# Kernel tuning notes

Hardware: AMD Instinct MI355X
Metric: run time of the kernel (lower is better)

The kernel has to match this reference:

```python
import jax, jax.numpy as jnp
import numpy as np

BS, NS, NSTEP = 128, 1024, 8
IN_DIM, HID, MLP = 768, 512, 512
NEG = -100000.0


def setup_inputs() -> dict:
    key = jax.random.key(0)
    ks = jax.random.split(key, 12)
    s_h = 1.0 / np.sqrt(HID)
    s_cat = 1.0 / np.sqrt(HID + IN_DIM)
    s_m = 1.0 / np.sqrt(MLP)
    # gumbel noise implements Categorical sampling as argmax(logits + gumbel)
    u = jax.random.uniform(ks[9], (NSTEP, BS, NS), jnp.float32, 1e-7, 1.0 - 1e-7)
    return {
        "target_emb": jax.random.normal(ks[0], (BS, IN_DIM), jnp.float32),
        "ctx_emb": jax.random.normal(ks[1], (BS, NS, IN_DIM), jnp.float32),
        "target_len": jax.random.randint(ks[2], (BS,), 1, 32),
        "ctx_len": jax.random.randint(ks[3], (BS,), NSTEP, NS + 1),
        "n_step": NSTEP,
        "W_ih": jax.random.normal(ks[4], (4 * HID, IN_DIM), jnp.float32) * s_h,
        "W_hh": jax.random.normal(ks[5], (4 * HID, HID), jnp.float32) * s_h,
        "b_ih": jnp.zeros((4 * HID,), jnp.float32),
        "b_hh": jnp.zeros((4 * HID,), jnp.float32),
        "W1c": jax.random.normal(ks[6], (MLP, IN_DIM), jnp.float32) * s_cat,
        "W1h": jax.random.normal(ks[7], (MLP, HID), jnp.float32) * s_cat,
        "b1": jnp.zeros((MLP,), jnp.float32),
        "w2": jax.random.normal(ks[8], (MLP,), jnp.float32) * s_m,
        "b2": jnp.zeros((), jnp.float32),
        "gumbel": -jnp.log(-jnp.log(u)),
    }


def reference(target_emb, ctx_emb, target_len, ctx_len, n_step,
              W_ih, W_hh, b_ih, b_hh, W1c, W1h, b1, w2, b2, gumbel):
    bs, ns, in_dim = ctx_emb.shape
    hid = W_hh.shape[1]
    # mlp1 split: ctx part is constant across steps (concat([ctx, h]) @ W1^T = ctx@W1c^T + h@W1h^T)
    ctx_part = jnp.einsum('bnd,md->bnm', ctx_emb, W1c) + b1  # [bs, ns, mlp]
    mask0 = jnp.where(jnp.arange(ns)[None, :] >= ctx_len[:, None], NEG, 0.0).astype(jnp.float32)
    h0 = jnp.zeros((bs, hid), jnp.float32)
    c0 = jnp.zeros((bs, hid), jnp.float32)
    lp0 = jnp.zeros((bs,), jnp.float32)
    batch_idx = jnp.arange(bs)

    def step(carry, g):
        h, c, mask, x, lp = carry
        # LSTMCell (torch gate order: i, f, g, o); dropout is identity (eval semantics)
        gates = x @ W_ih.T + b_ih + h @ W_hh.T + b_hh
        i_g, f_g, g_g, o_g = jnp.split(gates, 4, axis=-1)
        c_new = jax.nn.sigmoid(f_g) * c + jax.nn.sigmoid(i_g) * jnp.tanh(g_g)
        h_new = jax.nn.sigmoid(o_g) * jnp.tanh(c_new)
        # attention-style MLP score
        pre = ctx_part + (h_new @ W1h.T)[:, None, :]          # [bs, ns, mlp]
        sc = jnp.tanh(pre) @ w2 + b2 + mask                   # [bs, ns]
        # Categorical(probs=softmax(sc)).sample() via Gumbel-argmax
        out = jnp.argmax(sc + g, axis=-1)                     # [bs]
        lp = lp + jnp.take_along_axis(jax.nn.log_softmax(sc, axis=-1), out[:, None], 1)[:, 0]
        mask = mask.at[batch_idx, out].set(NEG)
        x_new = jnp.take_along_axis(ctx_emb, out[:, None, None], axis=1)[:, 0, :]
        return (h_new, c_new, mask, x_new, lp), out

    (h, c, mask, x, log_probs), outputs = jax.lax.scan(
        step, (h0, c0, mask0, target_emb, lp0), gumbel)
    return outputs, log_probs
```

## Files before the change

### kernel.cpp

```cpp
#include <hip/hip_runtime.h>
#include <hip/hip_bf16.h>

#define BSZ 128
#define NSQ 1024
#define NSTEPC 8
#define IND 768
#define HIDD 512
#define G4D 2048
#define MLPD 512
#define NEGV -100000.0f
#define KSGATE 4
#define MSPLIT 4

typedef __attribute__((ext_vector_type(4))) float f32x4;
typedef __attribute__((ext_vector_type(8))) short short8v;

__device__ __forceinline__ void gl16(const unsigned short* g, unsigned short* l) {
  __builtin_amdgcn_global_load_lds(
      (const __attribute__((address_space(1))) unsigned int*)(g),
      (__attribute__((address_space(3))) unsigned int*)(l), 16, 0, 0);
}

__device__ __forceinline__ void split2(float4 f0, float4 f1, short8v& hi, short8v& lo) {
  float fv[8] = {f0.x, f0.y, f0.z, f0.w, f1.x, f1.y, f1.z, f1.w};
#pragma unroll
  for (int j = 0; j < 8; ++j) {
    const unsigned ub = __builtin_bit_cast(unsigned, fv[j]);
    const unsigned hb = ub & 0xFFFF0000u;
    const float lf = fv[j] - __builtin_bit_cast(float, hb);
    hi[j] = (short)(hb >> 16);
    lo[j] = (short)(__builtin_bit_cast(unsigned, lf) >> 16);
  }
}

__device__ __forceinline__ float tanh_fast(float x) {
  x = fminf(fmaxf(x, -15.0f), 15.0f);
  float e = __builtin_amdgcn_exp2f(x * 2.8853900817779268f);
  float r = __builtin_amdgcn_rcpf(e + 1.0f);
  return fmaf(-2.0f, r, 1.0f);
}

__global__ __launch_bounds__(256) void k_prep_w(
    const float* __restrict__ W1c, const float* __restrict__ W_ih,
    const float* __restrict__ W_hh,
    unsigned short* __restrict__ wch, unsigned short* __restrict__ wcl,
    unsigned short* __restrict__ wgh, unsigned short* __restrict__ wgl) {
  int c = blockIdx.x * 256 + threadIdx.x;
  const float* src;
  unsigned short *dh, *dl;
  size_t unit;
  if (c < 49152) {
    const int row = c / 96, wc = c - row * 96;
    const int tile = wc >> 2, c4 = wc & 3;
    const int slot = c4 ^ ((row >> 1) & 3);
    unit = ((size_t)((row >> 7) * 24 + tile) * 128 + (row & 127)) * 4 + slot;
    src = W1c + (size_t)row * IND + wc * 8;
    dh = wch; dl = wcl;
  } else {
    c -= 49152;
    if (c >= 327680) return;
    const int row = c / 160, wc = c - row * 160;
    const int k0 = wc * 8;
    const int tile = wc >> 2, c4 = wc & 3;
    const int slot = c4 ^ ((row >> 1) & 3);
    unit = ((size_t)((row >> 7) * 40 + tile) * 128 + (row & 127)) * 4 + slot;
    src = (k0 < IND) ? (W_ih + (size_t)row * IND + k0)
                     : (W_hh + (size_t)row * HIDD + (k0 - IND));
    dh = wgh; dl = wgl;
  }
  const float4 f0 = *(const float4*)src, f1 = *(const float4*)(src + 4);
  short8v hi, lo;
  split2(f0, f1, hi, lo);
  *(short8v*)(dh + unit * 8) = hi;
  *(short8v*)(dl + unit * 8) = lo;
}

__global__ __launch_bounds__(256) void k_init2(
    const float* __restrict__ te, const int* __restrict__ cl,
    float* __restrict__ mask, float* __restrict__ cst, float* __restrict__ lp,
    unsigned short* __restrict__ xhh, unsigned short* __restrict__ xhl) {
  const int b = blockIdx.x, tid = threadIdx.x;
  const int L = cl[b];
  for (int n = tid; n < NSQ; n += 256) mask[(size_t)b * NSQ + n] = (n >= L) ? NEGV : 0.0f;
  for (int j = tid; j < HIDD; j += 256) cst[(size_t)b * HIDD + j] = 0.0f;
  if (tid == 0) lp[b] = 0.0f;
  if (tid < 160) {
    const int tile = tid >> 2, c4 = tid & 3;
    const int slot = c4 ^ ((b >> 1) & 3);
    const size_t ub = (((size_t)tile * 128 + b) * 4 + slot) * 8;
    short8v hi = {}, lo = {};
    if (tid < 96) {
      const float* s = te + (size_t)b * IND + tid * 8;
      split2(*(const float4*)s, *(const float4*)(s + 4), hi, lo);
    }
    *(short8v*)&xhh[ub] = hi;
    *(short8v*)&xhl[ub] = lo;
  }
}

__global__ __launch_bounds__(256) void k_ctx2(
    const float* __restrict__ ctx,
    const unsigned short* __restrict__ wch, const unsigned short* __restrict__ wcl,
    const float* __restrict__ bias, const int* __restrict__ clen,
    float* __restrict__ cp) {
  __shared__ __align__(16) unsigned short sWh[8192], sWl[8192];
  __shared__ __align__(16) unsigned short sCh[2048], sCl[2048];
  const int i0 = blockIdx.y * 64;
  const int b = i0 >> 10;
  const int nbase = i0 & 1023;
  if (nbase >= clen[b]) return;
  const int m0 = blockIdx.x * 256;
  const int rb0 = blockIdx.x * 2;
  const int tid = threadIdx.x;
  const int lane = tid & 63, wid = tid >> 6;
  const int l15 = lane & 15, l4 = lane >> 4;
  const int crow = tid >> 2, cc4 = tid & 3;
  const int ckread = cc4 ^ ((crow >> 1) & 3);
  const float* csrc = ctx + (size_t)(i0 + crow) * IND + ckread * 8;

  f32x4 acc[4][4] = {};
  for (int t = 0; t < 24; ++t) {
#pragma unroll
    for (int i = 0; i < 8; ++i) {
      const int v = wid * 1024 + i * 4096;
      const int plane = v >> 14;
      const int rem = v & 16383;
      const int rbh = rem >> 13;
      const int offs = (rem & 8191) >> 1;
      const unsigned short* g = (plane ? wcl : wch) +
          ((size_t)((rb0 + rbh) * 24 + t)) * 4096 + offs + lane * 8;
      unsigned short* l = (plane ? sWl : sWh) + rbh * 4096 + offs;
      gl16(g, l);
    }
    {
      const float* s = csrc + t * 32;
      short8v hi, lo;
      split2(*(const float4*)s, *(const float4*)(s + 4), hi, lo);
      *(short8v*)&sCh[tid * 8] = hi;
      *(short8v*)&sCl[tid * 8] = lo;
    }
    __syncthreads();
    short8v ah[4], al[4], bh[4], bl[4];
#pragma unroll
    for (int f = 0; f < 4; ++f) {
      const int rw = wid * 64 + f * 16 + l15;
      const int sw = l4 ^ ((rw >> 1) & 3);
      ah[f] = *(const short8v*)&sWh[rw * 32 + sw * 8];
      al[f] = *(const short8v*)&sWl[rw * 32 + sw * 8];
      const int rc = f * 16 + l15;
      const int sc = l4 ^ ((rc >> 1) & 3);
      bh[f] = *(const short8v*)&sCh[rc * 32 + sc * 8];
      bl[f] = *(const short8v*)&sCl[rc * 32 + sc * 8];
    }
#pragma unroll
    for (int fm = 0; fm < 4; ++fm)
#pragma unroll
      for (int fn = 0; fn < 4; ++fn) {
        acc[fm][fn] = __builtin_amdgcn_mfma_f32_16x16x32_bf16(ah[fm], bh[fn], acc[fm][fn], 0, 0, 0);
        acc[fm][fn] = __builtin_amdgcn_mfma_f32_16x16x32_bf16(ah[fm], bl[fn], acc[fm][fn], 0, 0, 0);
        acc[fm][fn] = __builtin_amdgcn_mfma_f32_16x16x32_bf16(al[fm], bh[fn], acc[fm][fn], 0, 0, 0);
      }
    __syncthreads();
  }
#pragma unroll
  for (int fm = 0; fm < 4; ++fm) {
#pragma unroll
    for (int r = 0; r < 4; ++r) {
      const int m = m0 + wid * 64 + fm * 16 + l4 * 4 + r;
      const float bb = bias[m];
      float* dst = cp + (((size_t)(b * MLPD + m)) << 10) + nbase + l15;
#pragma unroll
      for (int fn = 0; fn < 4; ++fn)
        dst[fn * 16] = acc[fm][fn][r] + bb;
    }
  }
}

__global__ __launch_bounds__(256) void k_gates(
    const unsigned short* __restrict__ xhh, const unsigned short* __restrict__ xhl,
    const unsigned short* __restrict__ wgh, const unsigned short* __restrict__ wgl,
    float* __restrict__ gp) {
  __shared__ __align__(16) unsigned short sAh[4096], sAl[4096], sBh[4096], sBl[4096];
  const int nb = blockIdx.x;
  const int ks = blockIdx.y;
  const int tid = threadIdx.x;
  const int lane = tid & 63, wid = tid >> 6;
  const int wm = wid >> 1, wn = wid & 1;
  const int l15 = lane & 15, l4 = lane >> 4;
  f32x4 acc[4][4] = {};
  for (int t = 0; t < 10; ++t) {
    const int gt = ks * 10 + t;
#pragma unroll
    for (int i = 0; i < 8; ++i) {
      const int v = wid * 1024 + i * 4096;
      const int mm = v >> 13;
      const int offs = (v & 8191) >> 1;
      const unsigned short* g;
      unsigned short* l;
      if (mm == 0)      { g = xhh + (size_t)gt * 4096 + offs; l = sAh + offs; }
      else if (mm == 1) { g = xhl + (size_t)gt * 4096 + offs; l = sAl + offs; }
      else if (mm == 2) { g = wgh + ((size_t)nb * 40 + gt) * 4096 + offs; l = sBh + offs; }
      else              { g = wgl + ((size_t)nb * 40 + gt) * 4096 + offs; l = sBl + offs; }
      gl16(g + lane * 8, l);
    }
    __syncthreads();
    short8v ahv[4], alv[4], bhv[4], blv[4];
#pragma unroll
    for (int f = 0; f < 4; ++f) {
      const int ri = wm * 64 + f * 16 + l15;
      const int sa = l4 ^ ((ri >> 1) & 3);
      ahv[f] = *(const short8v*)&sAh[ri * 32 + sa * 8];
      alv[f] = *(const short8v*)&sAl[ri * 32 + sa * 8];
      const int rn = wn * 64 + f * 16 + l15;
      const int sb = l4 ^ ((rn >> 1) & 3);
      bhv[f] = *(const short8v*)&sBh[rn * 32 + sb * 8];
      blv[f] = *(const short8v*)&sBl[rn * 32 + sb * 8];
    }
#pragma unroll
    for (int fi = 0; fi < 4; ++fi)
#pragma unroll
      for (int fn = 0; fn < 4; ++fn) {
        acc[fi][fn] = __builtin_amdgcn_mfma_f32_16x16x32_bf16(ahv[fi], bhv[fn], acc[fi][fn], 0, 0, 0);
        acc[fi][fn] = __builtin_amdgcn_mfma_f32_16x16x32_bf16(ahv[fi], blv[fn], acc[fi][fn], 0, 0, 0);
        acc[fi][fn] = __builtin_amdgcn_mfma_f32_16x16x32_bf16(alv[fi], bhv[fn], acc[fi][fn], 0, 0, 0);
      }
    __syncthreads();
  }
#pragma unroll
  for (int fi = 0; fi < 4; ++fi) {
#pragma unroll
    for (int r = 0; r < 4; ++r) {
      const int i = wm * 64 + fi * 16 + l4 * 4 + r;
      float* dst = gp + ((size_t)ks * BSZ + i) * G4D + nb * 128 + wn * 64 + l15;
#pragma unroll
      for (int fn = 0; fn < 4; ++fn)
        dst[fn * 16] = acc[fi][fn][r];
    }
  }
}

__global__ __launch_bounds__(512) void k_lstm2(
    const float* __restrict__ gp, const float* __restrict__ b_ih,
    const float* __restrict__ b_hh, const float* __restrict__ W1h,
    float* __restrict__ cst,
    unsigned short* __restrict__ xhh, unsigned short* __restrict__ xhl,
    float* __restrict__ hpp) {
  __shared__ float hs[HIDD];
  const int b = blockIdx.x, j = threadIdx.x;
  float g[4];
#pragma unroll
  for (int q = 0; q < 4; ++q) {
    float s = b_ih[q * HIDD + j] + b_hh[q * HIDD + j];
#pragma unroll
    for (int ks = 0; ks < KSGATE; ++ks)
      s += gp[((size_t)ks * BSZ + b) * G4D + q * HIDD + j];
    g[q] = s;
  }
  const float c_old = cst[(size_t)b * HIDD + j];
  const float ig = 1.0f / (1.0f + expf(-g[0]));
  const float fg = 1.0f / (1.0f + expf(-g[1]));
  const float gg = tanhf(g[2]);
  const float og = 1.0f / (1.0f + expf(-g[3]));
  const float cn = fg * c_old + ig * gg;
  const float hn = og * tanhf(cn);
  cst[(size_t)b * HIDD + j] = cn;
  hs[j] = hn;
  {
    const int tile = 24 + (j >> 5);
    const int c4 = (j >> 3) & 3;
    const int slot = c4 ^ ((b >> 1) & 3);
    const size_t u16i = (((size_t)tile * 128 + b) * 4 + slot) * 8 + (j & 7);
    const unsigned ubh = __builtin_bit_cast(unsigned, hn) & 0xFFFF0000u;
    const float lf = hn - __builtin_bit_cast(float, ubh);
    xhh[u16i] = (unsigned short)(ubh >> 16);
    xhl[u16i] = (unsigned short)(__builtin_bit_cast(unsigned, lf) >> 16);
  }
  __syncthreads();
  const float* wr = W1h + (size_t)j * HIDD;
  float s = 0.0f;
#pragma unroll 4
  for (int k = 0; k < HIDD; k += 4) {
    const float4 h4 = *(const float4*)&hs[k];
    const float4 w4 = *(const float4*)&wr[k];
    s = fmaf(h4.x, w4.x, fmaf(h4.y, w4.y, fmaf(h4.z, w4.z, fmaf(h4.w, w4.w, s))));
  }
  hpp[(size_t)b * HIDD + j] = s;
}

__global__ __launch_bounds__(256) void k_scores(
    const float* __restrict__ cp, const float* __restrict__ hpp,
    const float* __restrict__ w2, const int* __restrict__ clen,
    float* __restrict__ psc) {
  const int mh = blockIdx.x;
  const int b = blockIdx.y;
  const int tid = threadIdx.x;
  __shared__ float hsm[128], wsm[128];
  if (tid < 128) {
    hsm[tid] = hpp[(size_t)b * MLPD + mh * 128 + tid];
    wsm[tid] = w2[mh * 128 + tid];
  }
  __syncthreads();
  const int len = clen[b];
  const int n0 = tid * 4;
  if (n0 >= len) return;
  float ax = 0, ay = 0, az = 0, aw = 0;
  const float* base = cp + ((size_t)b * MLPD + mh * 128) * NSQ + n0;
#pragma unroll 4
  for (int mm = 0; mm < 128; ++mm) {
    const float4 c4 = *(const float4*)(base + (size_t)mm * NSQ);
    const float h = hsm[mm], w = wsm[mm];
    ax = fmaf(tanh_fast(c4.x + h), w, ax);
    ay = fmaf(tanh_fast(c4.y + h), w, ay);
    az = fmaf(tanh_fast(c4.z + h), w, az);
    aw = fmaf(tanh_fast(c4.w + h), w, aw);
  }
  *(float4*)(psc + ((size_t)b * MSPLIT + mh) * NSQ + n0) = make_float4(ax, ay, az, aw);
}

__global__ __launch_bounds__(256) void k_argmax(
    const float* __restrict__ psc, float* __restrict__ mask,
    const float* __restrict__ gum, const float* __restrict__ b2p,
    float* __restrict__ lp, const float* __restrict__ ctx,
    unsigned short* __restrict__ xhh, unsigned short* __restrict__ xhl,
    float* __restrict__ outv, int step) {
  const int b = blockIdx.x, tid = threadIdx.x;
  __shared__ float rv[256], rs[256], rm[256];
  __shared__ int ri[256];
  __shared__ int sel;
  const float b2 = b2p[0];
  const int n0 = tid * 4;
  const float4 m4 = *(const float4*)(mask + (size_t)b * NSQ + n0);
  float sc[4] = {b2 + m4.x, b2 + m4.y, b2 + m4.z, b2 + m4.w};
#pragma unroll
  for (int mh = 0; mh < MSPLIT; ++mh) {
    const float4 p4 = *(const float4*)(psc + ((size_t)b * MSPLIT + mh) * NSQ + n0);
    sc[0] += p4.x; sc[1] += p4.y; sc[2] += p4.z; sc[3] += p4.w;
  }
  const float4 g4 = *(const float4*)(gum + ((size_t)step * BSZ + b) * NSQ + n0);
  const float gv[4] = {g4.x, g4.y, g4.z, g4.w};
  float bestv = -1e30f, bests = 0.0f, msc = -1e30f;
  int bestn = 0;
#pragma unroll
  for (int q = 0; q < 4; ++q) {
    const float v = sc[q] + gv[q];
    if (v > bestv) { bestv = v; bestn = n0 + q; bests = sc[q]; }
    msc = fmaxf(msc, sc[q]);
  }
  rv[tid] = bestv; ri[tid] = bestn; rs[tid] = bests; rm[tid] = msc;
  __syncthreads();
  for (int o = 128; o > 0; o >>= 1) {
    if (tid < o) {
      if (rv[tid + o] > rv[tid] || (rv[tid + o] == rv[tid] && ri[tid + o] < ri[tid])) {
        rv[tid] = rv[tid + o]; ri[tid] = ri[tid + o]; rs[tid] = rs[tid + o];
      }
      rm[tid] = fmaxf(rm[tid], rm[tid + o]);
    }
    __syncthreads();
  }
  const float M = rm[0];
  __syncthreads();
  float se = 0.0f;
#pragma unroll
  for (int q = 0; q < 4; ++q)
    se += __builtin_amdgcn_exp2f((sc[q] - M) * 1.4426950408889634f);
  rm[tid] = se;
  __syncthreads();
  for (int o = 128; o > 0; o >>= 1) {
    if (tid < o) rm[tid] += rm[tid + o];
    __syncthreads();
  }
  if (tid == 0) {
    const int n = ri[0];
    const float lse = M + logf(rm[0]);
    const float nlp = lp[b] + rs[0] - lse;
    lp[b] = nlp;
    mask[(size_t)b * NSQ + n] = NEGV;
    outv[step * BSZ + b] = (float)n;
    if (step == NSTEPC - 1) outv[NSTEPC * BSZ + b] = nlp;
    sel = n;
  }
  __syncthreads();
  const int n = sel;
  if (tid < 96) {
    const float* src = ctx + ((size_t)b * NSQ + n) * IND + tid * 8;
    const int tile = tid >> 2, c4 = tid & 3;
    const int slot = c4 ^ ((b >> 1) & 3);
    const size_t ub = (((size_t)tile * 128 + b) * 4 + slot) * 8;
    short8v hi, lo;
    split2(*(const float4*)src, *(const float4*)(src + 4), hi, lo);
    *(short8v*)&xhh[ub] = hi;
    *(short8v*)&xhl[ub] = lo;
  }
}

extern "C" void kernel_launch(void* const* d_in, const int* in_sizes, int n_in,
                              void* d_out, int out_size, void* d_ws, size_t ws_size,
                              hipStream_t stream) {
  const float* target_emb = (const float*)d_in[0];
  const float* ctx_emb   = (const float*)d_in[1];
  const int*   ctx_len   = (const int*)d_in[3];
  const float* W_ih = (const float*)d_in[5];
  const float* W_hh = (const float*)d_in[6];
  const float* b_ih = (const float*)d_in[7];
  const float* b_hh = (const float*)d_in[8];
  const float* W1c  = (const float*)d_in[9];
  const float* W1h  = (const float*)d_in[10];
  const float* b1   = (const float*)d_in[11];
  const float* w2   = (const float*)d_in[12];
  const float* b2   = (const float*)d_in[13];
  const float* gumbel = (const float*)d_in[14];
  float* out = (float*)d_out;

  float* ws = (float*)d_ws;
  size_t off = 0;
  auto alloc = [&](size_t n) { float* p = ws + off; off += (n + 63) & ~(size_t)63; return p; };

  float* cp   = alloc((size_t)BSZ * MLPD * NSQ);
  float* gp   = alloc((size_t)KSGATE * BSZ * G4D);
  float* hpp  = alloc((size_t)BSZ * MLPD);
  float* psc  = alloc((size_t)BSZ * MSPLIT * NSQ);
  float* mask = alloc((size_t)BSZ * NSQ);
  float* cst  = alloc((size_t)BSZ * HIDD);
  float* lp   = alloc(128);
  unsigned short* wch = (unsigned short*)alloc(196608);
  unsigned short* wcl = (unsigned short*)alloc(196608);
  unsigned short* wgh = (unsigned short*)alloc(1310720);
  unsigned short* wgl = (unsigned short*)alloc(1310720);
  unsigned short* xhh = (unsigned short*)alloc(81920);
  unsigned short* xhl = (unsigned short*)alloc(81920);

  k_prep_w<<<1472, 256, 0, stream>>>(W1c, W_ih, W_hh, wch, wcl, wgh, wgl);
  k_init2<<<BSZ, 256, 0, stream>>>(target_emb, ctx_len, mask, cst, lp, xhh, xhl);
  k_ctx2<<<dim3(2, 2048), 256, 0, stream>>>(ctx_emb, wch, wcl, b1, ctx_len, cp);

  for (int t = 0; t < NSTEPC; ++t) {
    k_gates<<<dim3(16, KSGATE), 256, 0, stream>>>(xhh, xhl, wgh, wgl, gp);
    k_lstm2<<<BSZ, 512, 0, stream>>>(gp, b_ih, b_hh, W1h, cst, xhh, xhl, hpp);
    k_scores<<<dim3(MSPLIT, BSZ), 256, 0, stream>>>(cp, hpp, w2, ctx_len, psc);
    k_argmax<<<BSZ, 256, 0, stream>>>(psc, mask, gumbel, b2, lp, ctx_emb, xhh, xhl, out, t);
  }
}
```

Before: 953.8 us.

## Fuse score and argmax kernels, enlarge ctx GEMM tile, double gate split-K

Merges the per-step score and argmax kernels into one launch. The last of the MSPLIT blocks for each batch row, found with an atomic counter and threadfence, performs the reduction, sampling and mask update. The ctx projection GEMM moves to 512-thread blocks covering 128 context rows, so each W1c tile loaded into LDS is reused twice as much. The gate GEMM split-K factor goes from 4 to 8 for more parallelism, at the cost of more partial sums for the LSTM kernel to reduce. The fusion removes eight launches but relies on correct memory fencing and counter reset.

```diff
diff --git a/kernel.cpp b/kernel.cpp
--- a/kernel.cpp
+++ b/kernel.cpp
@@ -9,7 +9,7 @@
 #define G4D 2048
 #define MLPD 512
 #define NEGV -100000.0f
-#define KSGATE 4
+#define KSGATE 8
 #define MSPLIT 4
 
 typedef __attribute__((ext_vector_type(4))) float f32x4;
@@ -78,12 +78,13 @@
 __global__ __launch_bounds__(256) void k_init2(
     const float* __restrict__ te, const int* __restrict__ cl,
     float* __restrict__ mask, float* __restrict__ cst, float* __restrict__ lp,
+    int* __restrict__ cnt,
     unsigned short* __restrict__ xhh, unsigned short* __restrict__ xhl) {
   const int b = blockIdx.x, tid = threadIdx.x;
   const int L = cl[b];
   for (int n = tid; n < NSQ; n += 256) mask[(size_t)b * NSQ + n] = (n >= L) ? NEGV : 0.0f;
   for (int j = tid; j < HIDD; j += 256) cst[(size_t)b * HIDD + j] = 0.0f;
-  if (tid == 0) lp[b] = 0.0f;
+  if (tid == 0) { lp[b] = 0.0f; cnt[b] = 0; }
   if (tid < 160) {
     const int tile = tid >> 2, c4 = tid & 3;
     const int slot = c4 ^ ((b >> 1) & 3);
@@ -98,21 +99,22 @@
   }
 }
 
-__global__ __launch_bounds__(256) void k_ctx2(
+__global__ __launch_bounds__(512) void k_ctx3(
     const float* __restrict__ ctx,
     const unsigned short* __restrict__ wch, const unsigned short* __restrict__ wcl,
     const float* __restrict__ bias, const int* __restrict__ clen,
     float* __restrict__ cp) {
   __shared__ __align__(16) unsigned short sWh[8192], sWl[8192];
-  __shared__ __align__(16) unsigned short sCh[2048], sCl[2048];
-  const int i0 = blockIdx.y * 64;
-  const int b = i0 >> 10;
+  __shared__ __align__(16) unsigned short sCh[4096], sCl[4096];
+  const int i0 = blockIdx.y * 128;
+  const int b = blockIdx.y >> 3;
   const int nbase = i0 & 1023;
   if (nbase >= clen[b]) return;
   const int m0 = blockIdx.x * 256;
   const int rb0 = blockIdx.x * 2;
   const int tid = threadIdx.x;
   const int lane = tid & 63, wid = tid >> 6;
+  const int wm = wid & 3, wn = wid >> 2;
   const int l15 = lane & 15, l4 = lane >> 4;
   const int crow = tid >> 2, cc4 = tid & 3;
   const int ckread = cc4 ^ ((crow >> 1) & 3);
@@ -121,15 +123,13 @@
   f32x4 acc[4][4] = {};
   for (int t = 0; t < 24; ++t) {
 #pragma unroll
-    for (int i = 0; i < 8; ++i) {
-      const int v = wid * 1024 + i * 4096;
-      const int plane = v >> 14;
-      const int rem = v & 16383;
-      const int rbh = rem >> 13;
-      const int offs = (rem & 8191) >> 1;
-      const unsigned short* g = (plane ? wcl : wch) +
-          ((size_t)((rb0 + rbh) * 24 + t)) * 4096 + offs + lane * 8;
-      unsigned short* l = (plane ? sWl : sWh) + rbh * 4096 + offs;
+    for (int i = 0; i < 4; ++i) {
+      const int s = wid * 4 + i;
+      const int p = s >> 4, q = s & 15;
+      const int rbh = q >> 3;
+      const unsigned short* g = (p ? wcl : wch) +
+          ((size_t)((rb0 + rbh) * 24 + t)) * 4096 + (q & 7) * 512 + lane * 8;
+      unsigned short* l = (p ? sWl : sWh) + q * 512;
       gl16(g, l);
     }
     {
@@ -143,11 +143,11 @@
     short8v ah[4], al[4], bh[4], bl[4];
 #pragma unroll
     for (int f = 0; f < 4; ++f) {
-      const int rw = wid * 64 + f * 16 + l15;
+      const int rw = wm * 64 + f * 16 + l15;
       const int sw = l4 ^ ((rw >> 1) & 3);
       ah[f] = *(const short8v*)&sWh[rw * 32 + sw * 8];
       al[f] = *(const short8v*)&sWl[rw * 32 + sw * 8];
-      const int rc = f * 16 + l15;
+      const int rc = wn * 64 + f * 16 + l15;
       const int sc = l4 ^ ((rc >> 1) & 3);
       bh[f] = *(const short8v*)&sCh[rc * 32 + sc * 8];
       bl[f] = *(const short8v*)&sCl[rc * 32 + sc * 8];
@@ -166,9 +166,9 @@
   for (int fm = 0; fm < 4; ++fm) {
 #pragma unroll
     for (int r = 0; r < 4; ++r) {
-      const int m = m0 + wid * 64 + fm * 16 + l4 * 4 + r;
+      const int m = m0 + wm * 64 + fm * 16 + l4 * 4 + r;
       const float bb = bias[m];
-      float* dst = cp + (((size_t)(b * MLPD + m)) << 10) + nbase + l15;
+      float* dst = cp + (((size_t)(b * MLPD + m)) << 10) + nbase + wn * 64 + l15;
 #pragma unroll
       for (int fn = 0; fn < 4; ++fn)
         dst[fn * 16] = acc[fm][fn][r] + bb;
@@ -188,8 +188,8 @@
   const int wm = wid >> 1, wn = wid & 1;
   const int l15 = lane & 15, l4 = lane >> 4;
   f32x4 acc[4][4] = {};
-  for (int t = 0; t < 10; ++t) {
-    const int gt = ks * 10 + t;
+  for (int t = 0; t < 5; ++t) {
+    const int gt = ks * 5 + t;
 #pragma unroll
     for (int i = 0; i < 8; ++i) {
       const int v = wid * 1024 + i * 4096;
@@ -287,53 +287,59 @@
   hpp[(size_t)b * HIDD + j] = s;
 }
 
-__global__ __launch_bounds__(256) void k_scores(
+__global__ __launch_bounds__(256) void k_scoremax(
     const float* __restrict__ cp, const float* __restrict__ hpp,
     const float* __restrict__ w2, const int* __restrict__ clen,
-    float* __restrict__ psc) {
+    float* __restrict__ psc, int* __restrict__ cnt,
+    float* __restrict__ mask, const float* __restrict__ gum,
+    const float* __restrict__ b2p, float* __restrict__ lp,
+    const float* __restrict__ ctx,
+    unsigned short* __restrict__ xhh, unsigned short* __restrict__ xhl,
+    float* __restrict__ outv, int step) {
   const int mh = blockIdx.x;
   const int b = blockIdx.y;
   const int tid = threadIdx.x;
   __shared__ float hsm[128], wsm[128];
+  __shared__ float rv[256], rs[256], rm[256];
+  __shared__ int ri[256];
+  __shared__ int lastFlag, sel;
+  const int len = clen[b];
   if (tid < 128) {
     hsm[tid] = hpp[(size_t)b * MLPD + mh * 128 + tid];
     wsm[tid] = w2[mh * 128 + tid];
   }
   __syncthreads();
-  const int len = clen[b];
   const int n0 = tid * 4;
-  if (n0 >= len) return;
-  float ax = 0, ay = 0, az = 0, aw = 0;
-  const float* base = cp + ((size_t)b * MLPD + mh * 128) * NSQ + n0;
+  if (n0 < len) {
+    float ax = 0, ay = 0, az = 0, aw = 0;
+    const float* base = cp + ((size_t)b * MLPD + mh * 128) * NSQ + n0;
 #pragma unroll 4
-  for (int mm = 0; mm < 128; ++mm) {
-    const float4 c4 = *(const float4*)(base + (size_t)mm * NSQ);
-    const float h = hsm[mm], w = wsm[mm];
-    ax = fmaf(tanh_fast(c4.x + h), w, ax);
-    ay = fmaf(tanh_fast(c4.y + h), w, ay);
-    az = fmaf(tanh_fast(c4.z + h), w, az);
-    aw = fmaf(tanh_fast(c4.w + h), w, aw);
-  }
-  *(float4*)(psc + ((size_t)b * MSPLIT + mh) * NSQ + n0) = make_float4(ax, ay, az, aw);
-}
-
-__global__ __launch_bounds__(256) void k_argmax(
-    const float* __restrict__ psc, float* __restrict__ mask,
-    const float* __restrict__ gum, const float* __restrict__ b2p,
-    float* __restrict__ lp, const float* __restrict__ ctx,
-    unsigned short* __restrict__ xhh, unsigned short* __restrict__ xhl,
-    float* __restrict__ outv, int step) {
-  const int b = blockIdx.x, tid = threadIdx.x;
-  __shared__ float rv[256], rs[256], rm[256];
-  __shared__ int ri[256];
-  __shared__ int sel;
+    for (int mm = 0; mm < 128; ++mm) {
+      const float4 c4 = *(const float4*)(base + (size_t)mm * NSQ);
+      const float h = hsm[mm], w = wsm[mm];
+      ax = fmaf(tanh_fast(c4.x + h), w, ax);
+      ay = fmaf(tanh_fast(c4.y + h), w, ay);
+      az = fmaf(tanh_fast(c4.z + h), w, az);
+      aw = fmaf(tanh_fast(c4.w + h), w, aw);
+    }
+    *(float4*)(psc + ((size_t)b * MSPLIT + mh) * NSQ + n0) = make_float4(ax, ay, az, aw);
+  }
+  __threadfence();
+  __syncthreads();
+  if (tid == 0) {
+    const int old = atomicAdd(&cnt[b], 1);
+    lastFlag = (old == MSPLIT - 1);
+  }
+  __syncthreads();
+  if (!lastFlag) return;
+  __threadfence();
+
   const float b2 = b2p[0];
-  const int n0 = tid * 4;
   const float4 m4 = *(const float4*)(mask + (size_t)b * NSQ + n0);
   float sc[4] = {b2 + m4.x, b2 + m4.y, b2 + m4.z, b2 + m4.w};
 #pragma unroll
-  for (int mh = 0; mh < MSPLIT; ++mh) {
-    const float4 p4 = *(const float4*)(psc + ((size_t)b * MSPLIT + mh) * NSQ + n0);
+  for (int q = 0; q < MSPLIT; ++q) {
+    const float4 p4 = *(const float4*)(psc + ((size_t)b * MSPLIT + q) * NSQ + n0);
     sc[0] += p4.x; sc[1] += p4.y; sc[2] += p4.z; sc[3] += p4.w;
   }
   const float4 g4 = *(const float4*)(gum + ((size_t)step * BSZ + b) * NSQ + n0);
@@ -378,6 +384,7 @@
     outv[step * BSZ + b] = (float)n;
     if (step == NSTEPC - 1) outv[NSTEPC * BSZ + b] = nlp;
     sel = n;
+    cnt[b] = 0;
   }
   __syncthreads();
   const int n = sel;
@@ -422,6 +429,7 @@
   float* mask = alloc((size_t)BSZ * NSQ);
   float* cst  = alloc((size_t)BSZ * HIDD);
   float* lp   = alloc(128);
+  int*   cnt  = (int*)alloc(128);
   unsigned short* wch = (unsigned short*)alloc(196608);
   unsigned short* wcl = (unsigned short*)alloc(196608);
   unsigned short* wgh = (unsigned short*)alloc(1310720);
@@ -430,13 +438,14 @@
   unsigned short* xhl = (unsigned short*)alloc(81920);
 
   k_prep_w<<<1472, 256, 0, stream>>>(W1c, W_ih, W_hh, wch, wcl, wgh, wgl);
-  k_init2<<<BSZ, 256, 0, stream>>>(target_emb, ctx_len, mask, cst, lp, xhh, xhl);
-  k_ctx2<<<dim3(2, 2048), 256, 0, stream>>>(ctx_emb, wch, wcl, b1, ctx_len, cp);
+  k_init2<<<BSZ, 256, 0, stream>>>(target_emb, ctx_len, mask, cst, lp, cnt, xhh, xhl);
+  k_ctx3<<<dim3(2, 1024), 512, 0, stream>>>(ctx_emb, wch, wcl, b1, ctx_len, cp);
 
   for (int t = 0; t < NSTEPC; ++t) {
     k_gates<<<dim3(16, KSGATE), 256, 0, stream>>>(xhh, xhl, wgh, wgl, gp);
     k_lstm2<<<BSZ, 512, 0, stream>>>(gp, b_ih, b_hh, W1h, cst, xhh, xhl, hpp);
-    k_scores<<<dim3(MSPLIT, BSZ), 256, 0, stream>>>(cp, hpp, w2, ctx_len, psc);
-    k_argmax<<<BSZ, 256, 0, stream>>>(psc, mask, gumbel, b2, lp, ctx_emb, xhh, xhl, out, t);
-  }
-}
+    k_scoremax<<<dim3(MSPLIT, BSZ), 256, 0, stream>>>(
+        cp, hpp, w2, ctx_len, psc, cnt, mask, gumbel, b2, lp,
+        ctx_emb, xhh, xhl, out, t);
+  }
+}
```

After: 1.625 ms. 1.7x slower.

## Pre-split context embeddings to bf16 planes and use 128x128 ctx GEMM tiles

Applied to the files above, without the earlier changes.

Adds a pass that converts ctx_emb into swizzled bf16 hi/lo planes once, so the context projection GEMM can stream both operands via global_load_lds into square 128x128 tiles instead of splitting fp32 on the fly. It also doubles the K-split of the gates GEMM to launch more blocks per step. The cost is an extra workspace buffer the size of ctx_emb and an extra full read/write pass over it, and more partial gate sums to reduce. The new path runs only if the workspace is large enough.

```diff
diff --git a/kernel.cpp b/kernel.cpp
--- a/kernel.cpp
+++ b/kernel.cpp
@@ -9,7 +9,7 @@
 #define G4D 2048
 #define MLPD 512
 #define NEGV -100000.0f
-#define KSGATE 4
+#define KSGATE 8
 #define MSPLIT 4
 
 typedef __attribute__((ext_vector_type(4))) float f32x4;
@@ -75,6 +75,30 @@
   *(short8v*)(dl + unit * 8) = lo;
 }
 
+__global__ __launch_bounds__(256) void k_prep_ctx(
+    const float* __restrict__ ctx, const int* __restrict__ clen,
+    unsigned short* __restrict__ cxh, unsigned short* __restrict__ cxl) {
+  const int rb = blockIdx.x;
+  const int b = rb >> 3;
+  const int nbase = (rb & 7) << 7;
+  if (nbase >= clen[b]) return;
+  const int tid = threadIdx.x;
+  const float* src = ctx + (size_t)rb * 128 * IND;
+  for (int it = 0; it < 48; ++it) {
+    const int cc = it * 256 + tid;
+    const int row = (int)(((unsigned)cc * 21846u) >> 21);
+    const int wc = cc - row * 96;
+    const int t = wc >> 2, c4 = wc & 3;
+    const int slot = c4 ^ ((row >> 1) & 3);
+    const size_t u = (((size_t)(rb * 24 + t)) * 128 + row) * 4 + slot;
+    const float* s = src + (size_t)row * IND + wc * 8;
+    short8v hi, lo;
+    split2(*(const float4*)s, *(const float4*)(s + 4), hi, lo);
+    *(short8v*)(cxh + u * 8) = hi;
+    *(short8v*)(cxl + u * 8) = lo;
+  }
+}
+
 __global__ __launch_bounds__(256) void k_init2(
     const float* __restrict__ te, const int* __restrict__ cl,
     float* __restrict__ mask, float* __restrict__ cst, float* __restrict__ lp,
@@ -95,6 +119,68 @@
     }
     *(short8v*)&xhh[ub] = hi;
     *(short8v*)&xhl[ub] = lo;
+  }
+}
+
+__global__ __launch_bounds__(256) void k_ctx4(
+    const unsigned short* __restrict__ cxh, const unsigned short* __restrict__ cxl,
+    const unsigned short* __restrict__ wch, const unsigned short* __restrict__ wcl,
+    const float* __restrict__ bias, const int* __restrict__ clen,
+    float* __restrict__ cp) {
+  __shared__ __align__(16) unsigned short sWh[4096], sWl[4096], sCh[4096], sCl[4096];
+  const int rbC = blockIdx.y;
+  const int b = rbC >> 3;
+  const int nbase = (rbC & 7) << 7;
+  if (nbase >= clen[b]) return;
+  const int rbW = blockIdx.x;
+  const int m0 = rbW << 7;
+  const int tid = threadIdx.x;
+  const int lane = tid & 63, wid = tid >> 6;
+  const int wm = wid & 1, wn = wid >> 1;
+  const int l15 = lane & 15, l4 = lane >> 4;
+  unsigned short* sP = (wid == 0) ? sWh : (wid == 1) ? sWl : (wid == 2) ? sCh : sCl;
+  const unsigned short* gP = (wid == 0) ? wch : (wid == 1) ? wcl : (wid == 2) ? cxh : cxl;
+  const size_t gBase = ((size_t)((wid < 2) ? rbW : rbC) * 24) * 4096 + lane * 8;
+
+  f32x4 acc[4][4] = {};
+  for (int t = 0; t < 24; ++t) {
+#pragma unroll
+    for (int q = 0; q < 8; ++q)
+      gl16(gP + gBase + t * 4096 + q * 512, sP + q * 512);
+    __syncthreads();
+    short8v ah[4], al[4], bh[4], bl[4];
+#pragma unroll
+    for (int f = 0; f < 4; ++f) {
+      const int rw = wm * 64 + f * 16 + l15;
+      const int so = (l4 ^ ((rw >> 1) & 3)) << 3;
+      ah[f] = *(const short8v*)&sWh[rw * 32 + so];
+      al[f] = *(const short8v*)&sWl[rw * 32 + so];
+      const int rc = wn * 64 + f * 16 + l15;
+      const int sc = (l4 ^ ((rc >> 1) & 3)) << 3;
+      bh[f] = *(const short8v*)&sCh[rc * 32 + sc];
+      bl[f] = *(const short8v*)&sCl[rc * 32 + sc];
+    }
+#pragma unroll
+    for (int fm = 0; fm < 4; ++fm)
+#pragma unroll
+      for (int fn = 0; fn < 4; ++fn) {
+        acc[fm][fn] = __builtin_amdgcn_mfma_f32_16x16x32_bf16(ah[fm], bh[fn], acc[fm][fn], 0, 0, 0);
+        acc[fm][fn] = __builtin_amdgcn_mfma_f32_16x16x32_bf16(ah[fm], bl[fn], acc[fm][fn], 0, 0, 0);
+        acc[fm][fn] = __builtin_amdgcn_mfma_f32_16x16x32_bf16(al[fm], bh[fn], acc[fm][fn], 0, 0, 0);
+      }
+    __syncthreads();
+  }
+#pragma unroll
+  for (int fm = 0; fm < 4; ++fm) {
+#pragma unroll
+    for (int r = 0; r < 4; ++r) {
+      const int m = m0 + wm * 64 + fm * 16 + l4 * 4 + r;
+      const float bb = bias[m];
+      float* dst = cp + (((size_t)(b * MLPD + m)) << 10) + nbase + wn * 64 + l15;
+#pragma unroll
+      for (int fn = 0; fn < 4; ++fn)
+        dst[fn * 16] = acc[fm][fn][r] + bb;
+    }
   }
 }
 
@@ -117,7 +203,6 @@
   const int crow = tid >> 2, cc4 = tid & 3;
   const int ckread = cc4 ^ ((crow >> 1) & 3);
   const float* csrc = ctx + (size_t)(i0 + crow) * IND + ckread * 8;
-
   f32x4 acc[4][4] = {};
   for (int t = 0; t < 24; ++t) {
 #pragma unroll
@@ -188,8 +273,8 @@
   const int wm = wid >> 1, wn = wid & 1;
   const int l15 = lane & 15, l4 = lane >> 4;
   f32x4 acc[4][4] = {};
-  for (int t = 0; t < 10; ++t) {
-    const int gt = ks * 10 + t;
+  for (int t = 0; t < 5; ++t) {
+    const int gt = ks * 5 + t;
 #pragma unroll
     for (int i = 0; i < 8; ++i) {
       const int v = wid * 1024 + i * 4096;
@@ -428,10 +513,24 @@
   unsigned short* wgl = (unsigned short*)alloc(1310720);
   unsigned short* xhh = (unsigned short*)alloc(81920);
   unsigned short* xhl = (unsigned short*)alloc(81920);
+  const size_t ctx_plane_elems = (size_t)BSZ * NSQ * IND / 2;
+  const bool presplit = ws_size >= (off + 2 * ((ctx_plane_elems + 63) & ~(size_t)63)) * 4;
+  unsigned short* cxh = nullptr; unsigned short* cxl = nullptr;
+  if (presplit) {
+    cxh = (unsigned short*)alloc(ctx_plane_elems);
+    cxl = (unsigned short*)alloc(ctx_plane_elems);
+  }
 
   k_prep_w<<<1472, 256, 0, stream>>>(W1c, W_ih, W_hh, wch, wcl, wgh, wgl);
   k_init2<<<BSZ, 256, 0, stream>>>(target_emb, ctx_len, mask, cst, lp, xhh, xhl);
-  k_ctx2<<<dim3(2, 2048), 256, 0, stream>>>(ctx_emb, wch, wcl, b1, ctx_len, cp);
+
+  if (presplit) {
+    k_prep_ctx<<<1024, 256, 0, stream>>>(ctx_emb, ctx_len, cxh, cxl);
+    k_ctx4<<<dim3(MLPD / 128, 1024), 256, 0, stream>>>(
+        cxh, cxl, wch, wcl, b1, ctx_len, cp);
+  } else {
+    k_ctx2<<<dim3(2, 2048), 256, 0, stream>>>(ctx_emb, wch, wcl, b1, ctx_len, cp);
+  }
 
   for (int t = 0; t < NSTEPC; ++t) {
     k_gates<<<dim3(16, KSGATE), 256, 0, stream>>>(xhh, xhl, wgh, wgl, gp);
```

New measurement: 1.056 ms. +10.7%, slower.
